# Optimization experiments

Hardware: AMD Instinct MI355X
Metric: run time of the kernel (lower is better)

Reference implementation:

```python
import jax, jax.numpy as jnp
import numpy as np

B, T, N, D = 2, 10, 1024, 1024
NH = 16
HD = D // NH


def setup_inputs() -> dict:
    key = jax.random.key(0)
    ks = jax.random.split(key, 9)
    data = jax.random.normal(ks[0], (B, N, D), jnp.float32)
    traj_pos = jax.random.normal(ks[1], (B, T, N, 3), jnp.float32)
    q = jax.random.normal(ks[2], (B, T, N, 4), jnp.float32)
    traj_quat = q / (jnp.linalg.norm(q, axis=-1, keepdims=True) + 1e-10)
    certainty = jax.random.uniform(ks[3], (B, N), jnp.float32)
    s = 1.0 / np.sqrt(D).astype(np.float32)
    Wq = jax.random.normal(ks[4], (D, D), jnp.float32) * s
    Wk = jax.random.normal(ks[5], (D, D), jnp.float32) * s
    Wv = jax.random.normal(ks[6], (D, D), jnp.float32) * s
    Wo = jax.random.normal(ks[7], (D, D), jnp.float32) * s
    z = jnp.zeros((D,), jnp.float32)
    return {"data": data, "traj_pos": traj_pos, "traj_quat": traj_quat,
            "certainty": certainty, "Wq": Wq, "bq": z, "Wk": Wk, "bk": z,
            "Wv": Wv, "bv": z, "Wo": Wo, "bo": z}


def reference(data, traj_pos, traj_quat, certainty, Wq, bq, Wk, bk, Wv, bv, Wo, bo):
    b, n, d = data.shape
    # --- trajectory similarity scores (same for all batches: torch.mean over batch+time) ---
    # pos_dist[i,j] = mean_{b,t} ||p_bti - p_btj||
    pd = jnp.linalg.norm(traj_pos[:, :, :, None, :] - traj_pos[:, :, None, :, :], axis=-1).mean(axis=(0, 1))  # (n,n)
    qdm = jnp.linalg.norm(traj_quat[:, :, :, None, :] - traj_quat[:, :, None, :, :], axis=-1).mean(axis=(0, 1))
    qdp = jnp.linalg.norm(traj_quat[:, :, :, None, :] + traj_quat[:, :, None, :, :], axis=-1).mean(axis=(0, 1))
    qd = jnp.minimum(qdm, qdp)
    traj = jnp.exp(-pd - qd)
    traj = traj / traj.sum(axis=-1, keepdims=True)  # (n,n) row-normalized

    def proj(x, W, bias):
        return (x @ W.T + bias).reshape(b, n, NH, HD).transpose(0, 2, 1, 3)  # (b,h,n,hd)

    Q = proj(data, Wq, bq)
    K = proj(data, Wk, bk)
    V = proj(data, Wv, bv)
    scores = jnp.einsum('bhid,bhjd->bhij', Q, K) / np.sqrt(HD).astype(np.float32)
    combined = scores + 0.5 * traj[None, None]  # broadcast over (batch, heads)
    attn = jax.nn.softmax(combined, axis=-1)
    out = jnp.einsum('bhij,bhjd->bhid', attn, V).transpose(0, 2, 1, 3).reshape(b, n, d)
    out = out @ Wo.T + bo
    # certainty update from attention entropy
    avg_attn = attn.mean(axis=1)  # (b,n,n)
    p = jnp.clip(avg_attn, 1e-10, None)
    Hent = -jnp.sum(p * jnp.log(p), axis=-1)  # (b,n)
    H_max = np.log(n).astype(np.float32)
    new_certainty = jnp.maximum(certainty, jax.nn.sigmoid(H_max - Hent))
    return out, new_certainty
```

## Files before the change

### kernel.cpp

```cpp
#include <hip/hip_runtime.h>
#include <math.h>

#define NB 2
#define NN 1024
#define DD 1024
#define NHH 16
#define HDD 64
#define BTT 20

typedef unsigned short u16;
typedef short bf16x8 __attribute__((ext_vector_type(8)));
typedef float f32x4 __attribute__((ext_vector_type(4)));

#define HMAXL 6.93147180559945f
#define C1 0.18033688011112042f
#define TLC 0.72134752044448170f
#define KC  0.072134752044448170f
#define CH 520

#define TRAJ_OFF 0
#define TL_OFF    1048576
#define DATAB_OFF 1572864
#define WQB_OFF   2621440
#define WKB_OFF   3145728
#define WVB_OFF   3670016
#define WOB_OFF   4194304
#define QB_OFF    4718592
#define KB_OFF    5767168
#define VT_OFF    6815744
#define AOB_OFF   7864320
#define LV_OFF    8912896
#define HPART_OFF 8945664
#define RSP_OFF   8978432

__device__ __forceinline__ float b2f(u16 h) { return __uint_as_float(((unsigned)h) << 16); }
__device__ __forceinline__ u16 f2bf(float f) {
  unsigned u = __float_as_uint(f);
  return (u16)((u + 0x7fffu + ((u >> 16) & 1u)) >> 16);
}
__device__ __forceinline__ void dma16(const void* g, void* l) {
  __builtin_amdgcn_global_load_lds((const __attribute__((address_space(1))) void*)g,
                                   (__attribute__((address_space(3))) void*)l, 16, 0, 0);
}

__global__ __launch_bounds__(256) void prep_kernel(const float* __restrict__ data,
                                                   const float* __restrict__ w0,
                                                   const float* __restrict__ w1,
                                                   const float* __restrict__ w2,
                                                   const float* __restrict__ w3,
                                                   u16* __restrict__ dd,
                                                   u16* __restrict__ d0, u16* __restrict__ d1,
                                                   u16* __restrict__ d2, u16* __restrict__ d3,
                                                   const float* __restrict__ pos,
                                                   const float* __restrict__ quat,
                                                   float* __restrict__ w,
                                                   float* __restrict__ rsp) {
  const int tid = threadIdx.x;
  const int bid = blockIdx.x;
  __shared__ float ld[8][BTT][8];
  __shared__ float wredS[4][8];
  if (bid >= 512) {
    int cb = bid - 512;
    int z = cb >> 10;
    const float* s;
    u16* d;
    size_t off = 0;
    if (z < 2) { s = data; d = dd; off = (size_t)z * 1048576; }
    else if (z == 2) { s = w0; d = d0; }
    else if (z == 3) { s = w1; d = d1; }
    else if (z == 4) { s = w2; d = d2; }
    else { s = w3; d = d3; }
    size_t i = off + (size_t)((cb & 1023) * 256 + tid) * 4;
    float4 v = *(const float4*)(s + i);
    ushort4 o = {f2bf(v.x), f2bf(v.y), f2bf(v.z), f2bf(v.w)};
    *(ushort4*)(d + i) = o;
    return;
  }
  const int jx = bid & 3;
  const int j = jx * 256 + tid;
  const int i0 = (bid >> 2) * 8;
  if (tid < 8 * BTT) {
    int ii = tid / BTT, bt = tid % BTT;
    const float* pp = pos + ((size_t)bt * NN + i0 + ii) * 3;
    ld[ii][bt][0] = pp[0]; ld[ii][bt][1] = pp[1]; ld[ii][bt][2] = pp[2];
    *(float4*)&ld[ii][bt][4] = *(const float4*)(quat + ((size_t)bt * NN + i0 + ii) * 4);
  }
  __syncthreads();
  float acc[8] = {};
  for (int bt = 0; bt < BTT; ++bt) {
    const float* pj = pos + ((size_t)bt * NN + j) * 3;
    float pjx = pj[0], pjy = pj[1], pjz = pj[2];
    float4 qj = *(const float4*)(quat + ((size_t)bt * NN + j) * 4);
#pragma unroll
    for (int ii = 0; ii < 8; ++ii) {
      float4 pi = *(const float4*)&ld[ii][bt][0];
      float4 qi = *(const float4*)&ld[ii][bt][4];
      float dx = pi.x - pjx, dy = pi.y - pjy, dz = pi.z - pjz;
      float d2 = fmaf(dz, dz, fmaf(dy, dy, dx * dx));
      float dot = fmaf(qi.w, qj.w, fmaf(qi.z, qj.z, fmaf(qi.y, qj.y, qi.x * qj.x)));
      float tq = fmaf(-2.f, fabsf(dot), 2.f);
      acc[ii] += sqrtf(d2) + sqrtf(fmaxf(tq, 0.f));
    }
  }
  const int wv = tid >> 6;
#pragma unroll
  for (int ii = 0; ii < 8; ++ii) {
    float v = exp2f(-acc[ii] * KC);
    w[(size_t)(i0 + ii) * NN + j] = v;
    float s = v;
#pragma unroll
    for (int off = 1; off < 64; off <<= 1) s += __shfl_xor(s, off, 64);
    if ((tid & 63) == 0) wredS[wv][ii] = s;
  }
  __syncthreads();
  if (tid < 8)
    rsp[jx * 1024 + i0 + tid] = wredS[0][tid] + wredS[1][tid] + wredS[2][tid] + wredS[3][tid];
}

__global__ __launch_bounds__(256) void qkv_trajB_kernel(const u16* __restrict__ Ab,
                                                        const u16* __restrict__ Wq,
                                                        const u16* __restrict__ Wk,
                                                        const u16* __restrict__ Wv,
                                                        const float* __restrict__ bq,
                                                        const float* __restrict__ bk,
                                                        const float* __restrict__ bv,
                                                        u16* __restrict__ Qb,
                                                        u16* __restrict__ Kb,
                                                        u16* __restrict__ VtT,
                                                        const float* __restrict__ wtr,
                                                        const float* __restrict__ rsp,
                                                        u16* __restrict__ tl) {
  const int tid = threadIdx.x;
  __shared__ __align__(16) u16 As[128 * 32];
  __shared__ __align__(16) u16 Bs[128 * 32];
  if (blockIdx.x < 256) {
    int base = blockIdx.x * 4;
#pragma unroll
    for (int r = 0; r < 4; ++r) {
      int i = base + r;
      float inv = TLC / (rsp[i] + rsp[1024 + i] + rsp[2048 + i] + rsp[3072 + i]);
      float4 w4 = *(const float4*)(wtr + (size_t)i * NN + tid * 4);
      ushort4 o = {f2bf(w4.x * inv), f2bf(w4.y * inv), f2bf(w4.z * inv), f2bf(w4.w * inv)};
      *(ushort4*)(tl + (size_t)i * NN + tid * 4) = o;
    }
    return;
  }
  const int bid = blockIdx.x - 256;
  const int z = bid >> 7;
  const int rem = bid & 127;
  const int bxg = rem & 7, byg = rem >> 3;
  const u16* Wb = z == 0 ? Wq : (z == 1 ? Wk : Wv);
  const float* bias = z == 0 ? bq : (z == 1 ? bk : bv);
  const int w = tid >> 6, l = tid & 63, g = l >> 4, ln = l & 15;
  const int bm = byg << 7, bn = bxg << 7;
  const int srow = w * 16 + (l >> 2);
  const int scol = (l & 3) * 8;
  const u16* Ap0 = Ab + (size_t)(bm + srow) * DD + scol;
  const u16* Ap1 = Ab + (size_t)(bm + 64 + srow) * DD + scol;
  const u16* Bp0 = Wb + (size_t)(bn + srow) * DD + scol;
  const u16* Bp1 = Wb + (size_t)(bn + 64 + srow) * DD + scol;
  u16* dA0 = As + w * 512;
  u16* dA1 = As + 2048 + w * 512;
  u16* dB0 = Bs + w * 512;
  u16* dB1 = Bs + 2048 + w * 512;
  const int mw = (w & 1) * 64, nw = (w >> 1) * 64;
  f32x4 zero4 = {0.f, 0.f, 0.f, 0.f};
  f32x4 acc[4][4];
#pragma unroll
  for (int mt = 0; mt < 4; ++mt)
#pragma unroll
    for (int nt = 0; nt < 4; ++nt) acc[mt][nt] = zero4;
  for (int k0 = 0; k0 < DD; k0 += 32) {
    __syncthreads();
    dma16(Ap0 + k0, dA0); dma16(Ap1 + k0, dA1);
    dma16(Bp0 + k0, dB0); dma16(Bp1 + k0, dB1);
    __syncthreads();
    bf16x8 bfr[4], afr[4];
#pragma unroll
    for (int nt = 0; nt < 4; ++nt)
      bfr[nt] = *(const bf16x8*)&Bs[(nw + nt * 16 + ln) * 32 + g * 8];
#pragma unroll
    for (int mt = 0; mt < 4; ++mt)
      afr[mt] = *(const bf16x8*)&As[(mw + mt * 16 + ln) * 32 + g * 8];
#pragma unroll
    for (int mt = 0; mt < 4; ++mt)
#pragma unroll
      for (int nt = 0; nt < 4; ++nt)
        acc[mt][nt] = __builtin_amdgcn_mfma_f32_16x16x32_bf16(afr[mt], bfr[nt], acc[mt][nt], 0, 0, 0);
  }
#pragma unroll
  for (int nt = 0; nt < 4; ++nt) {
    int n = bn + nw + nt * 16 + ln;
    float bb = bias[n];
    if (z == 2) {
      int row = (((bm >> 10) << 4) + (n >> 6)) * 64 + (n & 63);
#pragma unroll
      for (int mt = 0; mt < 4; ++mt) {
        int tok = (bm & 1023) + mw + mt * 16 + g * 4;
        ushort4 pk = {f2bf(acc[mt][nt][0] + bb), f2bf(acc[mt][nt][1] + bb),
                      f2bf(acc[mt][nt][2] + bb), f2bf(acc[mt][nt][3] + bb)};
        *(ushort4*)(VtT + (size_t)row * NN + tok) = pk;
      }
    } else {
      u16* outp = z == 0 ? Qb : Kb;
#pragma unroll
      for (int mt = 0; mt < 4; ++mt) {
#pragma unroll
        for (int r = 0; r < 4; ++r) {
          int m = bm + mw + mt * 16 + g * 4 + r;
          outp[(size_t)m * DD + n] = f2bf(acc[mt][nt][r] + bb);
        }
      }
    }
  }
}

__global__ __launch_bounds__(256) void att_kernel(const u16* __restrict__ Qb,
                                                  const u16* __restrict__ Kb,
                                                  const u16* __restrict__ VtT,
                                                  const u16* __restrict__ tl,
                                                  u16* __restrict__ AOb,
                                                  float* __restrict__ Lv) {
  const int tid = threadIdx.x;
  const int bh = blockIdx.y;
  const int b = bh >> 4, h = bh & 15;
  const int i0 = blockIdx.x << 6;
  const int w = tid >> 6, l = tid & 63, g = l >> 4, ln = l & 15;
  const int wi0 = w * 16;
  __shared__ __align__(16) u16 Qs[8 * CH];
  __shared__ __align__(16) u16 Ks[2][8 * CH];
  __shared__ __align__(16) u16 Vts[2][8 * CH];
  __shared__ __align__(16) u16 Pt[64 * 72];
  __shared__ float lsc[64];
  const int c0 = 2 * w, c1 = 2 * w + 1;
  const int rr = 8 * (l >> 3);
  const int dcol = (l & 7) * 8;
  dma16(Qb + ((size_t)(b * NN) + i0 + c0 + rr) * DD + h * HDD + dcol, Qs + c0 * CH);
  dma16(Qb + ((size_t)(b * NN) + i0 + c1 + rr) * DD + h * HDD + dcol, Qs + c1 * CH);
  const int ig = i0 + wi0 + ln;
  const int lnlo = (ln & 7) * CH;
  const int lnhi = (ln >> 3) * 64;
  f32x4 zero4 = {0.f, 0.f, 0.f, 0.f};
  f32x4 oacc[4];
#pragma unroll
  for (int nt = 0; nt < 4; ++nt) oacc[nt] = zero4;
  float lacc = 0.f;
  for (int j0 = 0; j0 < NN; j0 += 128) {
    __syncthreads();
#pragma unroll
    for (int u = 0; u < 2; ++u) {
      int jb = j0 + u * 64;
      dma16(Kb + ((size_t)(b * NN) + jb + c0 + rr) * DD + h * HDD + dcol, Ks[u] + c0 * CH);
      dma16(Kb + ((size_t)(b * NN) + jb + c1 + rr) * DD + h * HDD + dcol, Ks[u] + c1 * CH);
      dma16(VtT + ((size_t)(bh * 64) + c0 + rr) * NN + jb + dcol, Vts[u] + c0 * CH);
      dma16(VtT + ((size_t)(bh * 64) + c1 + rr) * NN + jb + dcol, Vts[u] + c1 * CH);
    }
    ushort4 tlv[2][4];
#pragma unroll
    for (int u = 0; u < 2; ++u)
#pragma unroll
      for (int jt = 0; jt < 4; ++jt)
        tlv[u][jt] = *(const ushort4*)(tl + (size_t)ig * NN + j0 + u * 64 + jt * 16 + g * 4);
    __syncthreads();
    bf16x8 qf[2];
    qf[0] = *(const bf16x8*)&Qs[lnlo + (2 * w) * 64 + lnhi + g * 8];
    qf[1] = *(const bf16x8*)&Qs[lnlo + (2 * w) * 64 + lnhi + 32 + g * 8];
#pragma unroll
    for (int u = 0; u < 2; ++u) {
      f32x4 sacc[4];
      __builtin_amdgcn_s_setprio(1);
#pragma unroll
      for (int jt = 0; jt < 4; ++jt) {
        sacc[jt] = zero4;
#pragma unroll
        for (int kc = 0; kc < 2; ++kc) {
          bf16x8 af = *(const bf16x8*)&Ks[u][lnlo + (2 * jt) * 64 + lnhi + kc * 32 + g * 8];
          sacc[jt] = __builtin_amdgcn_mfma_f32_16x16x32_bf16(af, qf[kc], sacc[jt], 0, 0, 0);
        }
      }
      __builtin_amdgcn_s_setprio(0);
#pragma unroll
      for (int jt = 0; jt < 4; ++jt) {
        float e0 = exp2f(sacc[jt][0] * C1 + b2f(tlv[u][jt].x));
        float e1 = exp2f(sacc[jt][1] * C1 + b2f(tlv[u][jt].y));
        float e2 = exp2f(sacc[jt][2] * C1 + b2f(tlv[u][jt].z));
        float e3 = exp2f(sacc[jt][3] * C1 + b2f(tlv[u][jt].w));
        lacc += (e0 + e1) + (e2 + e3);
        ushort4 pk = {f2bf(e0), f2bf(e1), f2bf(e2), f2bf(e3)};
        *(ushort4*)(Pt + (wi0 + ln) * 72 + jt * 16 + g * 4) = pk;
      }
      bf16x8 pf[2];
      pf[0] = *(const bf16x8*)&Pt[(wi0 + ln) * 72 + g * 8];
      pf[1] = *(const bf16x8*)&Pt[(wi0 + ln) * 72 + 32 + g * 8];
      __builtin_amdgcn_s_setprio(1);
#pragma unroll
      for (int nt = 0; nt < 4; ++nt) {
#pragma unroll
        for (int kc = 0; kc < 2; ++kc) {
          bf16x8 vf = *(const bf16x8*)&Vts[u][lnlo + (2 * nt) * 64 + lnhi + kc * 32 + g * 8];
          oacc[nt] = __builtin_amdgcn_mfma_f32_16x16x32_bf16(pf[kc], vf, oacc[nt], 0, 0, 0);
        }
      }
      __builtin_amdgcn_s_setprio(0);
    }
  }
  lacc += __shfl_xor(lacc, 16, 64);
  lacc += __shfl_xor(lacc, 32, 64);
  if (g == 0) {
    Lv[(size_t)bh * NN + i0 + wi0 + ln] = lacc;
    lsc[wi0 + ln] = 1.f / lacc;
  }
  __syncthreads();
#pragma unroll
  for (int nt = 0; nt < 4; ++nt) {
    int d = nt * 16 + ln;
#pragma unroll
    for (int r = 0; r < 4; ++r) {
      int i = wi0 + g * 4 + r;
      float v = oacc[nt][r] * lsc[i];
      AOb[((size_t)(b * NN) + i0 + i) * DD + h * HDD + d] = f2bf(v);
    }
  }
}

__global__ __launch_bounds__(256) void ent_kernel(const u16* __restrict__ Qb,
                                                  const u16* __restrict__ Kb,
                                                  const u16* __restrict__ tl,
                                                  const float* __restrict__ Lv,
                                                  float* __restrict__ Hp) {
  const int tid = threadIdx.x;
  const int jx = blockIdx.x & 15;
  const int iy = (blockIdx.x >> 4) & 15;
  const int b = blockIdx.x >> 8;
  const int j0 = jx << 6, i0 = iy << 6;
  const int w = tid >> 6, l = tid & 63, g = l >> 4, ln = l & 15;
  const int wi0 = w * 16;
  __shared__ __align__(16) u16 Qs[32 * CH];
  __shared__ __align__(16) u16 Ks[32 * CH];
  __shared__ float linv[NHH * 64];
#pragma unroll
  for (int rep = 0; rep < 4; ++rep) {
    int idx = tid + (rep << 8);
    int hh = idx >> 6, ii = idx & 63;
    linv[hh * 64 + ii] = 1.f / Lv[((size_t)((b << 4) + hh)) * NN + i0 + ii];
  }
  const int rlo = l >> 5;
  const int scol = (l & 31) * 8;
  const int ig = i0 + wi0 + ln;
  const int elo = (ln >> 1) * CH;
  const int ehi = (ln & 1) * 256;
  ushort4 tlv[4];
#pragma unroll
  for (int jt = 0; jt < 4; ++jt)
    tlv[jt] = *(const ushort4*)(tl + (size_t)ig * NN + j0 + jt * 16 + g * 4);
  float P[4][4] = {};
  f32x4 zero4 = {0.f, 0.f, 0.f, 0.f};
  for (int hb = 0; hb < 4; ++hb) {
    __syncthreads();
#pragma unroll
    for (int cc = 0; cc < 8; ++cc) {
      int c = w * 8 + cc;
      dma16(Qb + ((size_t)(b * NN) + i0 + 2 * c + rlo) * DD + hb * 256 + scol, Qs + c * CH);
      dma16(Kb + ((size_t)(b * NN) + j0 + 2 * c + rlo) * DD + hb * 256 + scol, Ks + c * CH);
    }
    __syncthreads();
#pragma unroll
    for (int hl = 0; hl < 4; ++hl) {
      float li = linv[(hb * 4 + hl) * 64 + wi0 + ln];
      bf16x8 qf[2];
      qf[0] = *(const bf16x8*)&Qs[(w * 8) * CH + elo + ehi + hl * 64 + g * 8];
      qf[1] = *(const bf16x8*)&Qs[(w * 8) * CH + elo + ehi + hl * 64 + 32 + g * 8];
#pragma unroll
      for (int jt = 0; jt < 4; ++jt) {
        f32x4 sacc = zero4;
        __builtin_amdgcn_s_setprio(1);
#pragma unroll
        for (int kc = 0; kc < 2; ++kc) {
          bf16x8 af = *(const bf16x8*)&Ks[(jt * 8) * CH + elo + ehi + hl * 64 + kc * 32 + g * 8];
          sacc = __builtin_amdgcn_mfma_f32_16x16x32_bf16(af, qf[kc], sacc, 0, 0, 0);
        }
        __builtin_amdgcn_s_setprio(0);
        P[jt][0] += exp2f(sacc[0] * C1 + b2f(tlv[jt].x)) * li;
        P[jt][1] += exp2f(sacc[1] * C1 + b2f(tlv[jt].y)) * li;
        P[jt][2] += exp2f(sacc[2] * C1 + b2f(tlv[jt].z)) * li;
        P[jt][3] += exp2f(sacc[3] * C1 + b2f(tlv[jt].w)) * li;
      }
    }
  }
  float hs = 0.f;
#pragma unroll
  for (int jt = 0; jt < 4; ++jt) {
#pragma unroll
    for (int r = 0; r < 4; ++r) {
      float p = fmaxf(P[jt][r] * (1.f / NHH), 1e-10f);
      hs -= p * logf(p);
    }
  }
  hs += __shfl_xor(hs, 16, 64);
  hs += __shfl_xor(hs, 32, 64);
  if (g == 0) Hp[jx * 2048 + (size_t)b * NN + i0 + wi0 + ln] = hs;
}

__global__ __launch_bounds__(256) void gemmo_cert_kernel(const u16* __restrict__ Ab,
                                                         const u16* __restrict__ Wb,
                                                         const float* __restrict__ bias,
                                                         float* __restrict__ C,
                                                         const float* __restrict__ Hp,
                                                         const float* __restrict__ cert,
                                                         float* __restrict__ outc) {
  const int tid = threadIdx.x;
  __shared__ __align__(16) u16 As[128 * 32];
  __shared__ __align__(16) u16 Bs[64 * 32];
  if (blockIdx.x >= 256) {
    int idx = (blockIdx.x - 256) * 256 + tid;
    float H = 0.f;
#pragma unroll
    for (int jt = 0; jt < 16; ++jt) H += Hp[jt * 2048 + idx];
    float sg = 1.f / (1.f + expf(H - HMAXL));
    outc[idx] = fmaxf(cert[idx], sg);
    return;
  }
  const int bn = (blockIdx.x & 15) << 6;
  const int bm = (blockIdx.x >> 4) << 7;
  const int w = tid >> 6, l = tid & 63, g = l >> 4, ln = l & 15;
  const int srow = w * 16 + (l >> 2);
  const int scol = (l & 3) * 8;
  const u16* Ap0 = Ab + (size_t)(bm + srow) * DD + scol;
  const u16* Ap1 = Ab + (size_t)(bm + 64 + srow) * DD + scol;
  const u16* Bp0 = Wb + (size_t)(bn + srow) * DD + scol;
  u16* dA0 = As + w * 512;
  u16* dA1 = As + 2048 + w * 512;
  u16* dB0 = Bs + w * 512;
  const int mw = (w & 1) * 64, nw = (w >> 1) * 32;
  f32x4 zero4 = {0.f, 0.f, 0.f, 0.f};
  f32x4 acc[4][2];
#pragma unroll
  for (int mt = 0; mt < 4; ++mt)
#pragma unroll
    for (int nt = 0; nt < 2; ++nt) acc[mt][nt] = zero4;
  for (int k0 = 0; k0 < DD; k0 += 32) {
    __syncthreads();
    dma16(Ap0 + k0, dA0); dma16(Ap1 + k0, dA1);
    dma16(Bp0 + k0, dB0);
    __syncthreads();
    bf16x8 bfr[2], afr[4];
#pragma unroll
    for (int nt = 0; nt < 2; ++nt)
      bfr[nt] = *(const bf16x8*)&Bs[(nw + nt * 16 + ln) * 32 + g * 8];
#pragma unroll
    for (int mt = 0; mt < 4; ++mt)
      afr[mt] = *(const bf16x8*)&As[(mw + mt * 16 + ln) * 32 + g * 8];
#pragma unroll
    for (int mt = 0; mt < 4; ++mt)
#pragma unroll
      for (int nt = 0; nt < 2; ++nt)
        acc[mt][nt] = __builtin_amdgcn_mfma_f32_16x16x32_bf16(afr[mt], bfr[nt], acc[mt][nt], 0, 0, 0);
  }
#pragma unroll
  for (int nt = 0; nt < 2; ++nt) {
    int n = bn + nw + nt * 16 + ln;
    float bb = bias[n];
#pragma unroll
    for (int mt = 0; mt < 4; ++mt) {
#pragma unroll
      for (int r = 0; r < 4; ++r) {
        int m = bm + mw + mt * 16 + g * 4 + r;
        C[(size_t)m * DD + n] = acc[mt][nt][r] + bb;
      }
    }
  }
}

extern "C" void kernel_launch(void* const* d_in, const int* in_sizes, int n_in,
                              void* d_out, int out_size, void* d_ws, size_t ws_size,
                              hipStream_t stream) {
  const float* data      = (const float*)d_in[0];
  const float* traj_pos  = (const float*)d_in[1];
  const float* traj_quat = (const float*)d_in[2];
  const float* certainty = (const float*)d_in[3];
  const float* Wq = (const float*)d_in[4];
  const float* bq = (const float*)d_in[5];
  const float* Wk = (const float*)d_in[6];
  const float* bk = (const float*)d_in[7];
  const float* Wv = (const float*)d_in[8];
  const float* bv = (const float*)d_in[9];
  const float* Wo = (const float*)d_in[10];
  const float* bo = (const float*)d_in[11];

  float* ws = (float*)d_ws;
  float* wtr  = ws + TRAJ_OFF;
  u16* tl    = (u16*)(ws + TL_OFF);
  u16* datab = (u16*)(ws + DATAB_OFF);
  u16* wqb   = (u16*)(ws + WQB_OFF);
  u16* wkb   = (u16*)(ws + WKB_OFF);
  u16* wvb   = (u16*)(ws + WVB_OFF);
  u16* wob   = (u16*)(ws + WOB_OFF);
  u16* Qb    = (u16*)(ws + QB_OFF);
  u16* Kb    = (u16*)(ws + KB_OFF);
  u16* VtT   = (u16*)(ws + VT_OFF);
  u16* AOb   = (u16*)(ws + AOB_OFF);
  float* Lv   = ws + LV_OFF;
  float* Hp   = ws + HPART_OFF;
  float* rsp  = ws + RSP_OFF;
  float* out  = (float*)d_out;
  float* outc = out + (size_t)NB * NN * DD;

  prep_kernel<<<6656, 256, 0, stream>>>(data, Wq, Wk, Wv, Wo,
                                        datab, wqb, wkb, wvb, wob,
                                        traj_pos, traj_quat, wtr, rsp);
  qkv_trajB_kernel<<<640, 256, 0, stream>>>(datab, wqb, wkb, wvb, bq, bk, bv,
                                            Qb, Kb, VtT, wtr, rsp, tl);
  att_kernel<<<dim3(NN / 64, NB * NHH), 256, 0, stream>>>(Qb, Kb, VtT, tl, AOb, Lv);
  ent_kernel<<<512, 256, 0, stream>>>(Qb, Kb, tl, Lv, Hp);
  gemmo_cert_kernel<<<264, 256, 0, stream>>>(AOb, wob, bo, out, Hp, certainty, outc);
}
```

Before: 208.3 us.

## Double-buffer LDS tiles in QKV GEMM, attention and output GEMM kernels

Converts the QKV projection GEMM, the attention K/V loop and the output GEMM to ping-pong LDS buffers. The next tile's global-to-LDS copy is issued right after the barrier, while the current tile is computed. This leaves one barrier per iteration instead of two and is meant to hide load latency behind MFMA work. In exchange the GEMM kernels use twice the shared memory, which may lower occupancy. The attention loop now steps 64 keys at a time instead of 128, so it runs more iterations.

```diff
diff --git a/kernel.cpp b/kernel.cpp
--- a/kernel.cpp
+++ b/kernel.cpp
@@ -131,8 +131,8 @@
                                                         const float* __restrict__ rsp,
                                                         u16* __restrict__ tl) {
   const int tid = threadIdx.x;
-  __shared__ __align__(16) u16 As[128 * 32];
-  __shared__ __align__(16) u16 Bs[128 * 32];
+  __shared__ __align__(16) u16 As[2 * 128 * 32];
+  __shared__ __align__(16) u16 Bs[2 * 128 * 32];
   if (blockIdx.x < 256) {
     int base = blockIdx.x * 4;
 #pragma unroll
@@ -159,10 +159,6 @@
   const u16* Ap1 = Ab + (size_t)(bm + 64 + srow) * DD + scol;
   const u16* Bp0 = Wb + (size_t)(bn + srow) * DD + scol;
   const u16* Bp1 = Wb + (size_t)(bn + 64 + srow) * DD + scol;
-  u16* dA0 = As + w * 512;
-  u16* dA1 = As + 2048 + w * 512;
-  u16* dB0 = Bs + w * 512;
-  u16* dB1 = Bs + 2048 + w * 512;
   const int mw = (w & 1) * 64, nw = (w >> 1) * 64;
   f32x4 zero4 = {0.f, 0.f, 0.f, 0.f};
   f32x4 acc[4][4];
@@ -170,23 +166,33 @@
   for (int mt = 0; mt < 4; ++mt)
 #pragma unroll
     for (int nt = 0; nt < 4; ++nt) acc[mt][nt] = zero4;
-  for (int k0 = 0; k0 < DD; k0 += 32) {
+  auto stage = [&](int buf, int k0) {
+    u16* a = As + buf * 4096;
+    u16* bb = Bs + buf * 4096;
+    dma16(Ap0 + k0, a + w * 512); dma16(Ap1 + k0, a + 2048 + w * 512);
+    dma16(Bp0 + k0, bb + w * 512); dma16(Bp1 + k0, bb + 2048 + w * 512);
+  };
+  stage(0, 0);
+  int cur = 0;
+#pragma unroll 2
+  for (int t = 0; t < 32; ++t) {
     __syncthreads();
-    dma16(Ap0 + k0, dA0); dma16(Ap1 + k0, dA1);
-    dma16(Bp0 + k0, dB0); dma16(Bp1 + k0, dB1);
-    __syncthreads();
+    if (t < 31) stage(cur ^ 1, (t + 1) * 32);
+    const u16* Asc = As + cur * 4096;
+    const u16* Bsc = Bs + cur * 4096;
     bf16x8 bfr[4], afr[4];
 #pragma unroll
     for (int nt = 0; nt < 4; ++nt)
-      bfr[nt] = *(const bf16x8*)&Bs[(nw + nt * 16 + ln) * 32 + g * 8];
+      bfr[nt] = *(const bf16x8*)&Bsc[(nw + nt * 16 + ln) * 32 + g * 8];
 #pragma unroll
     for (int mt = 0; mt < 4; ++mt)
-      afr[mt] = *(const bf16x8*)&As[(mw + mt * 16 + ln) * 32 + g * 8];
+      afr[mt] = *(const bf16x8*)&Asc[(mw + mt * 16 + ln) * 32 + g * 8];
 #pragma unroll
     for (int mt = 0; mt < 4; ++mt)
 #pragma unroll
       for (int nt = 0; nt < 4; ++nt)
         acc[mt][nt] = __builtin_amdgcn_mfma_f32_16x16x32_bf16(afr[mt], bfr[nt], acc[mt][nt], 0, 0, 0);
+    cur ^= 1;
   }
 #pragma unroll
   for (int nt = 0; nt < 4; ++nt) {
@@ -240,69 +246,69 @@
   const int ig = i0 + wi0 + ln;
   const int lnlo = (ln & 7) * CH;
   const int lnhi = (ln >> 3) * 64;
+  auto stageKV = [&](int buf, int jb) {
+    dma16(Kb + ((size_t)(b * NN) + jb + c0 + rr) * DD + h * HDD + dcol, Ks[buf] + c0 * CH);
+    dma16(Kb + ((size_t)(b * NN) + jb + c1 + rr) * DD + h * HDD + dcol, Ks[buf] + c1 * CH);
+    dma16(VtT + ((size_t)(bh * 64) + c0 + rr) * NN + jb + dcol, Vts[buf] + c0 * CH);
+    dma16(VtT + ((size_t)(bh * 64) + c1 + rr) * NN + jb + dcol, Vts[buf] + c1 * CH);
+  };
+  stageKV(0, 0);
   f32x4 zero4 = {0.f, 0.f, 0.f, 0.f};
   f32x4 oacc[4];
 #pragma unroll
   for (int nt = 0; nt < 4; ++nt) oacc[nt] = zero4;
   float lacc = 0.f;
-  for (int j0 = 0; j0 < NN; j0 += 128) {
+  bf16x8 qf[2];
+  int cur = 0;
+#pragma unroll 2
+  for (int t = 0; t < 16; ++t) {
+    const int j0 = t << 6;
+    ushort4 tlv[4];
+#pragma unroll
+    for (int jt = 0; jt < 4; ++jt)
+      tlv[jt] = *(const ushort4*)(tl + (size_t)ig * NN + j0 + jt * 16 + g * 4);
     __syncthreads();
-#pragma unroll
-    for (int u = 0; u < 2; ++u) {
-      int jb = j0 + u * 64;
-      dma16(Kb + ((size_t)(b * NN) + jb + c0 + rr) * DD + h * HDD + dcol, Ks[u] + c0 * CH);
-      dma16(Kb + ((size_t)(b * NN) + jb + c1 + rr) * DD + h * HDD + dcol, Ks[u] + c1 * CH);
-      dma16(VtT + ((size_t)(bh * 64) + c0 + rr) * NN + jb + dcol, Vts[u] + c0 * CH);
-      dma16(VtT + ((size_t)(bh * 64) + c1 + rr) * NN + jb + dcol, Vts[u] + c1 * CH);
-    }
-    ushort4 tlv[2][4];
-#pragma unroll
-    for (int u = 0; u < 2; ++u)
-#pragma unroll
-      for (int jt = 0; jt < 4; ++jt)
-        tlv[u][jt] = *(const ushort4*)(tl + (size_t)ig * NN + j0 + u * 64 + jt * 16 + g * 4);
-    __syncthreads();
-    bf16x8 qf[2];
-    qf[0] = *(const bf16x8*)&Qs[lnlo + (2 * w) * 64 + lnhi + g * 8];
-    qf[1] = *(const bf16x8*)&Qs[lnlo + (2 * w) * 64 + lnhi + 32 + g * 8];
-#pragma unroll
-    for (int u = 0; u < 2; ++u) {
-      f32x4 sacc[4];
-      __builtin_amdgcn_s_setprio(1);
-#pragma unroll
-      for (int jt = 0; jt < 4; ++jt) {
-        sacc[jt] = zero4;
-#pragma unroll
-        for (int kc = 0; kc < 2; ++kc) {
-          bf16x8 af = *(const bf16x8*)&Ks[u][lnlo + (2 * jt) * 64 + lnhi + kc * 32 + g * 8];
-          sacc[jt] = __builtin_amdgcn_mfma_f32_16x16x32_bf16(af, qf[kc], sacc[jt], 0, 0, 0);
-        }
+    if (t < 15) stageKV(cur ^ 1, j0 + 64);
+    if (t == 0) {
+      qf[0] = *(const bf16x8*)&Qs[lnlo + (2 * w) * 64 + lnhi + g * 8];
+      qf[1] = *(const bf16x8*)&Qs[lnlo + (2 * w) * 64 + lnhi + 32 + g * 8];
+    }
+    f32x4 sacc[4];
+    __builtin_amdgcn_s_setprio(1);
+#pragma unroll
+    for (int jt = 0; jt < 4; ++jt) {
+      sacc[jt] = zero4;
+#pragma unroll
+      for (int kc = 0; kc < 2; ++kc) {
+        bf16x8 af = *(const bf16x8*)&Ks[cur][lnlo + (2 * jt) * 64 + lnhi + kc * 32 + g * 8];
+        sacc[jt] = __builtin_amdgcn_mfma_f32_16x16x32_bf16(af, qf[kc], sacc[jt], 0, 0, 0);
       }
-      __builtin_amdgcn_s_setprio(0);
-#pragma unroll
-      for (int jt = 0; jt < 4; ++jt) {
-        float e0 = exp2f(sacc[jt][0] * C1 + b2f(tlv[u][jt].x));
-        float e1 = exp2f(sacc[jt][1] * C1 + b2f(tlv[u][jt].y));
-        float e2 = exp2f(sacc[jt][2] * C1 + b2f(tlv[u][jt].z));
-        float e3 = exp2f(sacc[jt][3] * C1 + b2f(tlv[u][jt].w));
-        lacc += (e0 + e1) + (e2 + e3);
-        ushort4 pk = {f2bf(e0), f2bf(e1), f2bf(e2), f2bf(e3)};
-        *(ushort4*)(Pt + (wi0 + ln) * 72 + jt * 16 + g * 4) = pk;
+    }
+    __builtin_amdgcn_s_setprio(0);
+#pragma unroll
+    for (int jt = 0; jt < 4; ++jt) {
+      float e0 = exp2f(sacc[jt][0] * C1 + b2f(tlv[jt].x));
+      float e1 = exp2f(sacc[jt][1] * C1 + b2f(tlv[jt].y));
+      float e2 = exp2f(sacc[jt][2] * C1 + b2f(tlv[jt].z));
+      float e3 = exp2f(sacc[jt][3] * C1 + b2f(tlv[jt].w));
+      lacc += (e0 + e1) + (e2 + e3);
+      ushort4 pk = {f2bf(e0), f2bf(e1), f2bf(e2), f2bf(e3)};
+      *(ushort4*)(Pt + (wi0 + ln) * 72 + jt * 16 + g * 4) = pk;
+    }
+    bf16x8 pf[2];
+    pf[0] = *(const bf16x8*)&Pt[(wi0 + ln) * 72 + g * 8];
+    pf[1] = *(const bf16x8*)&Pt[(wi0 + ln) * 72 + 32 + g * 8];
+    __builtin_amdgcn_s_setprio(1);
+#pragma unroll
+    for (int nt = 0; nt < 4; ++nt) {
+#pragma unroll
+      for (int kc = 0; kc < 2; ++kc) {
+        bf16x8 vf = *(const bf16x8*)&Vts[cur][lnlo + (2 * nt) * 64 + lnhi + kc * 32 + g * 8];
+        oacc[nt] = __builtin_amdgcn_mfma_f32_16x16x32_bf16(pf[kc], vf, oacc[nt], 0, 0, 0);
       }
-      bf16x8 pf[2];
-      pf[0] = *(const bf16x8*)&Pt[(wi0 + ln) * 72 + g * 8];
-      pf[1] = *(const bf16x8*)&Pt[(wi0 + ln) * 72 + 32 + g * 8];
-      __builtin_amdgcn_s_setprio(1);
-#pragma unroll
-      for (int nt = 0; nt < 4; ++nt) {
-#pragma unroll
-        for (int kc = 0; kc < 2; ++kc) {
-          bf16x8 vf = *(const bf16x8*)&Vts[u][lnlo + (2 * nt) * 64 + lnhi + kc * 32 + g * 8];
-          oacc[nt] = __builtin_amdgcn_mfma_f32_16x16x32_bf16(pf[kc], vf, oacc[nt], 0, 0, 0);
-        }
-      }
-      __builtin_amdgcn_s_setprio(0);
-    }
+    }
+    __builtin_amdgcn_s_setprio(0);
+    cur ^= 1;
   }
   lacc += __shfl_xor(lacc, 16, 64);
   lacc += __shfl_xor(lacc, 32, 64);
@@ -409,8 +415,8 @@
                                                          const float* __restrict__ cert,
                                                          float* __restrict__ outc) {
   const int tid = threadIdx.x;
-  __shared__ __align__(16) u16 As[128 * 32];
-  __shared__ __align__(16) u16 Bs[64 * 32];
+  __shared__ __align__(16) u16 As[2 * 128 * 32];
+  __shared__ __align__(16) u16 Bs[2 * 64 * 32];
   if (blockIdx.x >= 256) {
     int idx = (blockIdx.x - 256) * 256 + tid;
     float H = 0.f;
@@ -428,9 +434,6 @@
   const u16* Ap0 = Ab + (size_t)(bm + srow) * DD + scol;
   const u16* Ap1 = Ab + (size_t)(bm + 64 + srow) * DD + scol;
   const u16* Bp0 = Wb + (size_t)(bn + srow) * DD + scol;
-  u16* dA0 = As + w * 512;
-  u16* dA1 = As + 2048 + w * 512;
-  u16* dB0 = Bs + w * 512;
   const int mw = (w & 1) * 64, nw = (w >> 1) * 32;
   f32x4 zero4 = {0.f, 0.f, 0.f, 0.f};
   f32x4 acc[4][2];
@@ -438,23 +441,33 @@
   for (int mt = 0; mt < 4; ++mt)
 #pragma unroll
     for (int nt = 0; nt < 2; ++nt) acc[mt][nt] = zero4;
-  for (int k0 = 0; k0 < DD; k0 += 32) {
+  auto stage = [&](int buf, int k0) {
+    u16* a = As + buf * 4096;
+    u16* bb = Bs + buf * 2048;
+    dma16(Ap0 + k0, a + w * 512); dma16(Ap1 + k0, a + 2048 + w * 512);
+    dma16(Bp0 + k0, bb + w * 512);
+  };
+  stage(0, 0);
+  int cur = 0;
+#pragma unroll 2
+  for (int t = 0; t < 32; ++t) {
     __syncthreads();
-    dma16(Ap0 + k0, dA0); dma16(Ap1 + k0, dA1);
-    dma16(Bp0 + k0, dB0);
-    __syncthreads();
+    if (t < 31) stage(cur ^ 1, (t + 1) * 32);
+    const u16* Asc = As + cur * 4096;
+    const u16* Bsc = Bs + cur * 2048;
     bf16x8 bfr[2], afr[4];
 #pragma unroll
     for (int nt = 0; nt < 2; ++nt)
-      bfr[nt] = *(const bf16x8*)&Bs[(nw + nt * 16 + ln) * 32 + g * 8];
+      bfr[nt] = *(const bf16x8*)&Bsc[(nw + nt * 16 + ln) * 32 + g * 8];
 #pragma unroll
     for (int mt = 0; mt < 4; ++mt)
-      afr[mt] = *(const bf16x8*)&As[(mw + mt * 16 + ln) * 32 + g * 8];
+      afr[mt] = *(const bf16x8*)&Asc[(mw + mt * 16 + ln) * 32 + g * 8];
 #pragma unroll
     for (int mt = 0; mt < 4; ++mt)
 #pragma unroll
       for (int nt = 0; nt < 2; ++nt)
         acc[mt][nt] = __builtin_amdgcn_mfma_f32_16x16x32_bf16(afr[mt], bfr[nt], acc[mt][nt], 0, 0, 0);
+    cur ^= 1;
   }
 #pragma unroll
   for (int nt = 0; nt < 2; ++nt) {
```

After: 212.5 us. No clear change (+2.0%).
